# Performance work log

Hardware: AMD Instinct MI355X
Metric: run time of the kernel (lower is better)

Reference implementation:

```python
import jax, jax.numpy as jnp
import numpy as np

B, L, N = 128, 4096, 256
MZ_MIN, MZ_MAX = 100.0, 1000.0
STD_DEV = 0.5 * (MZ_MAX - MZ_MIN) / N  # default std_dev from __init__
THRESH_LOW_WEIGHT = -10.0


def setup_inputs() -> dict:
    key = jax.random.key(0)
    k1, k2, k3 = jax.random.split(key, 3)
    # PeakSense.__init__: means = linspace(mz_min, mz_max, n_vals) + Normal(0, 0.5*std_dev)
    mu = jnp.linspace(MZ_MIN, MZ_MAX, N, dtype=jnp.float32) \
         + (0.5 * STD_DEV) * jax.random.normal(k1, (N,), dtype=jnp.float32)
    # log_vars filled with 2*log(std_dev)
    lv = jnp.full((N,), 2.0 * float(np.log(STD_DEV)), dtype=jnp.float32)
    # spectra: masses in [mz_min, mz_max] (sorted, as real centroided spectra are), positive intensities
    masses = MZ_MIN + (MZ_MAX - MZ_MIN) * jax.random.uniform(k2, (B, L), dtype=jnp.float32)
    masses = jnp.sort(masses, axis=1)
    intensities = jax.random.uniform(k3, (B, L), dtype=jnp.float32)
    return {"mu": mu, "lv": lv, "masses": masses, "intensities": intensities}


def reference(mu, lv, masses, intensities):
    # out[b, p] = sum_i exp(-0.5*(mz[b,i]-mu[p])^2 * exp(-lv[p])) * iv[b,i],
    # where terms with arg < THRESH_LOW_WEIGHT are dropped (kernel early-exit).
    inv_s2 = jnp.exp(-lv)                                  # [N], 1/sigma^2
    d = masses[:, :, None] - mu[None, None, :]             # [B, L, N]
    arg = (-0.5) * (d * d) * inv_s2                        # [B, L, N]
    w = jnp.where(arg >= THRESH_LOW_WEIGHT, jnp.exp(arg), jnp.zeros((), arg.dtype))
    return jnp.einsum('bln,bl->bn', w, intensities)        # [B, N]
```

## Files before the change

kernel.cpp:

```cpp
#include <hip/hip_runtime.h>
#include <math.h>


#define BLOCK 256
#define THRESH -10.0f

__global__ __launch_bounds__(BLOCK) void peaksense_kernel(
    const float* __restrict__ mu,
    const float* __restrict__ lv,
    const float* __restrict__ masses,
    const float* __restrict__ inten,
    float* __restrict__ out,
    int B, int L, int N)
{
    const int b    = blockIdx.y;
    const int i0   = blockIdx.x * BLOCK + threadIdx.x;
    const int lane = threadIdx.x & 63;
    const int wbase = blockIdx.x * BLOCK + (threadIdx.x & ~63);
    int nv = L - wbase;
    if (nv <= 0) return;
    if (nv > 64) nv = 64;

    const size_t rowoff = (size_t)b * L;
    const bool vload = (i0 < L);
    const float m  = vload ? masses[rowoff + i0] : INFINITY;
    const float iv = vload ? inten[rowoff + i0] : 0.0f;

    const float m_lo = __shfl(m, 0);
    const float m_hi = __shfl(m, nv - 1);

    float* __restrict__ outrow = out + (size_t)b * N;

    const int nk = (N + 63) / 64;
    for (int k = 0; k < nk; ++k) {
        const int pc = k * 64 + lane;
        float mu_l = 0.0f, nh_l = 0.0f;
        bool cand = false;
        if (pc < N) {
            mu_l = mu[pc];
            const float lvl = lv[pc];
            nh_l = -0.5f * __expf(-lvl);
            const float r = sqrtf(20.0f * __expf(lvl)) * 1.00001f + 1e-3f;
            cand = (mu_l + r >= m_lo) && (mu_l - r <= m_hi);
        }
        unsigned long long mask = __ballot(cand);
        while (mask) {
            const int s = (int)__builtin_ctzll(mask);
            mask &= mask - 1;
            const float mu_p = __shfl(mu_l, s);
            const float nh_p = __shfl(nh_l, s);
            const float d    = m - mu_p;
            const float arg  = d * d * nh_p;
            float t = (arg >= THRESH) ? __expf(arg) * iv : 0.0f;
            t += __shfl_xor(t, 1);
            t += __shfl_xor(t, 2);
            t += __shfl_xor(t, 4);
            t += __shfl_xor(t, 8);
            t += __shfl_xor(t, 16);
            t += __shfl_xor(t, 32);
            if (lane == 0)
                atomicAdd(&outrow[k * 64 + s], t);
        }
    }
}

extern "C" void kernel_launch(void* const* d_in, const int* in_sizes, int n_in,
                              void* d_out, int out_size, void* d_ws, size_t ws_size,
                              hipStream_t stream) {
    const float* mu     = (const float*)d_in[0];
    const float* lv     = (const float*)d_in[1];
    const float* masses = (const float*)d_in[2];
    const float* inten  = (const float*)d_in[3];
    float* out = (float*)d_out;

    const int N = in_sizes[0];
    const int B = out_size / N;
    const int L = in_sizes[2] / B;

    hipMemsetAsync(d_out, 0, (size_t)out_size * sizeof(float), stream);

    dim3 grid((L + BLOCK - 1) / BLOCK, B);
    peaksense_kernel<<<grid, BLOCK, 0, stream>>>(mu, lv, masses, inten, out, B, L, N);
}
```

Before: 70.47 us.

## Switch to per-peak gather with binary search over shared-memory sorted masses

Instead of having each wavefront of spectrum points ballot over candidate peaks and atomically add into the output, each block now stages a whole spectrum row in LDS. Two threads per peak binary-search the sorted masses for the window where the Gaussian argument can exceed the threshold, then sum only that range. This removes the atomics and the output memset. It assumes masses are sorted and L is at most MAXL=4096 (32 KB of LDS). Each spectrum row is now reloaded once per peak-group block (two blocks per row), and grid parallelism is limited to 2*B blocks.

```diff
diff --git a/kernel.cpp b/kernel.cpp
--- a/kernel.cpp
+++ b/kernel.cpp
@@ -3,6 +3,9 @@
 
 
 #define BLOCK 256
+#define SUB 2
+#define PPB (BLOCK / SUB)
+#define MAXL 4096
 #define THRESH -10.0f
 
 __global__ __launch_bounds__(BLOCK) void peaksense_kernel(
@@ -13,55 +16,55 @@
     float* __restrict__ out,
     int B, int L, int N)
 {
-    const int b    = blockIdx.y;
-    const int i0   = blockIdx.x * BLOCK + threadIdx.x;
-    const int lane = threadIdx.x & 63;
-    const int wbase = blockIdx.x * BLOCK + (threadIdx.x & ~63);
-    int nv = L - wbase;
-    if (nv <= 0) return;
-    if (nv > 64) nv = 64;
+    __shared__ float2 s[MAXL];
 
-    const size_t rowoff = (size_t)b * L;
-    const bool vload = (i0 < L);
-    const float m  = vload ? masses[rowoff + i0] : INFINITY;
-    const float iv = vload ? inten[rowoff + i0] : 0.0f;
+    const int pg = blockIdx.x;
+    const int b  = blockIdx.y;
+    const int t  = threadIdx.x;
 
-    const float m_lo = __shfl(m, 0);
-    const float m_hi = __shfl(m, nv - 1);
+    const float* __restrict__ mrow = masses + (size_t)b * L;
+    const float* __restrict__ irow = inten  + (size_t)b * L;
+    for (int i = t; i < L; i += BLOCK)
+        s[i] = make_float2(mrow[i], irow[i]);
+    __syncthreads();
 
-    float* __restrict__ outrow = out + (size_t)b * N;
+    const int lp  = t >> 1;
+    const int sub = t & 1;
+    const int p   = pg * PPB + lp;
+    if (p >= N) return;
 
-    const int nk = (N + 63) / 64;
-    for (int k = 0; k < nk; ++k) {
-        const int pc = k * 64 + lane;
-        float mu_l = 0.0f, nh_l = 0.0f;
-        bool cand = false;
-        if (pc < N) {
-            mu_l = mu[pc];
-            const float lvl = lv[pc];
-            nh_l = -0.5f * __expf(-lvl);
-            const float r = sqrtf(20.0f * __expf(lvl)) * 1.00001f + 1e-3f;
-            cand = (mu_l + r >= m_lo) && (mu_l - r <= m_hi);
-        }
-        unsigned long long mask = __ballot(cand);
-        while (mask) {
-            const int s = (int)__builtin_ctzll(mask);
-            mask &= mask - 1;
-            const float mu_p = __shfl(mu_l, s);
-            const float nh_p = __shfl(nh_l, s);
-            const float d    = m - mu_p;
-            const float arg  = d * d * nh_p;
-            float t = (arg >= THRESH) ? __expf(arg) * iv : 0.0f;
-            t += __shfl_xor(t, 1);
-            t += __shfl_xor(t, 2);
-            t += __shfl_xor(t, 4);
-            t += __shfl_xor(t, 8);
-            t += __shfl_xor(t, 16);
-            t += __shfl_xor(t, 32);
-            if (lane == 0)
-                atomicAdd(&outrow[k * 64 + s], t);
-        }
+    const float mu_p = mu[p];
+    const float lvp  = lv[p];
+    const float inv  = __expf(-lvp);
+    const float nh   = -0.5f * inv;
+    const float r    = sqrtf(20.0f / inv) * 1.00001f + 1e-3f;
+    const float tlo  = mu_p - r;
+    const float thi  = mu_p + r;
+
+    int lo = 0, hi = L;
+    while (lo < hi) {
+        int mid = (lo + hi) >> 1;
+        if (s[mid].x < tlo) lo = mid + 1; else hi = mid;
     }
+    const int start = lo;
+    int lo2 = start, hi2 = L;
+    while (lo2 < hi2) {
+        int mid = (lo2 + hi2) >> 1;
+        if (s[mid].x <= thi) lo2 = mid + 1; else hi2 = mid;
+    }
+    const int end = lo2;
+
+    float acc = 0.0f;
+    for (int i = start + sub; i < end; i += SUB) {
+        const float2 v = s[i];
+        const float d   = v.x - mu_p;
+        const float arg = d * d * nh;
+        if (arg >= THRESH)
+            acc += __expf(arg) * v.y;
+    }
+    acc += __shfl_xor(acc, 1);
+    if (sub == 0)
+        out[(size_t)b * N + p] = acc;
 }
 
 extern "C" void kernel_launch(void* const* d_in, const int* in_sizes, int n_in,
@@ -77,8 +80,7 @@
     const int B = out_size / N;
     const int L = in_sizes[2] / B;
 
-    hipMemsetAsync(d_out, 0, (size_t)out_size * sizeof(float), stream);
-
-    dim3 grid((L + BLOCK - 1) / BLOCK, B);
+    const int pgroups = (N + PPB - 1) / PPB;
+    dim3 grid(pgroups, B);
     peaksense_kernel<<<grid, BLOCK, 0, stream>>>(mu, lv, masses, inten, out, B, L, N);
 }
```

New measurement: 70.22 us. About the same (-0.4%).
